# Performance work log

Hardware: AMD Instinct MI355X
Metric: run time of the kernel (lower is better)

Reference implementation:

```python
import jax, jax.numpy as jnp
import numpy as np

EPS = 1e-5

def _ln(x, g, b):
    mu = jnp.mean(x, axis=-1, keepdims=True)
    var = jnp.var(x, axis=-1, keepdims=True)
    return (x - mu) * jax.lax.rsqrt(var + EPS) * g + b

def setup_inputs() -> dict:
    B, N, D, H = 8, 1024, 1024, 16
    hid = 4 * D
    key = jax.random.key(0)
    ks = jax.random.split(key, 16)
    s = lambda fan_in: 1.0 / np.sqrt(fan_in)
    return {
        "x": jax.random.normal(ks[0], (B, N, D), jnp.float32),
        "ln1_g": jnp.ones((D,), jnp.float32),
        "ln1_b": jnp.zeros((D,), jnp.float32),
        "qkv_w": jax.random.normal(ks[1], (D, 3 * D), jnp.float32) * s(D),
        "qkv_b": jnp.zeros((3 * D,), jnp.float32),
        "proj_w": jax.random.normal(ks[2], (D, D), jnp.float32) * s(D),
        "proj_b": jnp.zeros((D,), jnp.float32),
        "ls1_g": jnp.full((D,), 1e-5, jnp.float32),
        "ln2_g": jnp.ones((D,), jnp.float32),
        "ln2_b": jnp.zeros((D,), jnp.float32),
        "fc1_w": jax.random.normal(ks[3], (D, hid), jnp.float32) * s(D),
        "fc1_b": jnp.zeros((hid,), jnp.float32),
        "fc2_w": jax.random.normal(ks[4], (hid, D), jnp.float32) * s(hid),
        "fc2_b": jnp.zeros((D,), jnp.float32),
        "ls2_g": jnp.full((D,), 1e-5, jnp.float32),
    }

def reference(x, ln1_g, ln1_b, qkv_w, qkv_b, proj_w, proj_b, ls1_g,
              ln2_g, ln2_b, fc1_w, fc1_b, fc2_w, fc2_b, ls2_g):
    B, N, D = x.shape
    H = 16
    hd = D // H
    scale = hd ** -0.5
    # --- attention branch (pre-norm) ---
    h = _ln(x, ln1_g, ln1_b)
    qkv = h @ qkv_w + qkv_b                      # [B,N,3D]
    q, k, v = jnp.split(qkv, 3, axis=-1)
    reshape = lambda t: t.reshape(B, N, H, hd).transpose(0, 2, 1, 3)  # [B,H,N,hd]
    q, k, v = reshape(q), reshape(k), reshape(v)
    attn = jax.nn.softmax(jnp.einsum('bhnd,bhmd->bhnm', q, k) * scale, axis=-1)
    o = jnp.einsum('bhnm,bhmd->bhnd', attn, v)
    o = o.transpose(0, 2, 1, 3).reshape(B, N, D)
    o = o @ proj_w + proj_b
    x = x + ls1_g * o
    # --- MLP branch (pre-norm) ---
    h = _ln(x, ln2_g, ln2_b)
    h = jax.nn.gelu(h @ fc1_w + fc1_b, approximate=False)
    h = h @ fc2_w + fc2_b
    x = x + ls2_g * h
    return x
```

## Files before the change

### kernel.cpp

```cpp
#include <hip/hip_runtime.h>
#include <hip/hip_bf16.h>
#include <cstdint>

using u16 = unsigned short;
using u8 = unsigned char;
typedef __attribute__((ext_vector_type(8))) short bf16x8;
typedef __attribute__((ext_vector_type(4))) float f32x4;
typedef __attribute__((ext_vector_type(16))) float f32x16;
typedef __attribute__((ext_vector_type(8))) int i32x8;
typedef __attribute__((ext_vector_type(4))) u16 u16x4;

#define MFMA_BF16(a, b, c) __builtin_amdgcn_mfma_f32_16x16x32_bf16((a), (b), (c), 0, 0, 0)
#define MFMA_FP8(a, b, c) \
  __builtin_amdgcn_mfma_scale_f32_32x32x64_f8f6f4((a), (b), (c), 0, 0, 0, 0x7f7f7f7f, 0, 0x7f7f7f7f)

__device__ __forceinline__ u16 f2bf(float f) {
  __hip_bfloat16 h = __float2bfloat16(f);
  return __builtin_bit_cast(u16, h);
}

__device__ __forceinline__ u8 f2fp8(float a) {
  int r = __builtin_amdgcn_cvt_pk_fp8_f32(a, a, 0, false);
  return (u8)(r & 0xff);
}

__device__ __forceinline__ uint32_t f2fp8x4(float a, float b, float c, float d) {
  int r = __builtin_amdgcn_cvt_pk_fp8_f32(a, b, 0, false);
  r = __builtin_amdgcn_cvt_pk_fp8_f32(c, d, r, true);
  return (uint32_t)r;
}

__device__ __forceinline__ void gl_lds16(const void* gsrc, void* ldst) {
  __builtin_amdgcn_global_load_lds(
      (__attribute__((address_space(1))) void*)const_cast<void*>(gsrc),
      (__attribute__((address_space(3))) void*)ldst, 16, 0, 0);
}

__global__ __launch_bounds__(256) void transpose_conv8(const float* __restrict__ src,
                                                       u8* __restrict__ dst, int K, int N) {
  __shared__ float t[32][33];
  const int bx = blockIdx.x, by = blockIdx.y;
  const int tid = threadIdx.x;
  const int r = tid >> 3, c = (tid & 7) * 4;
  const float4 v = *(const float4*)&src[(size_t)(by * 32 + r) * N + bx * 32 + c];
  t[r][c] = v.x; t[r][c + 1] = v.y; t[r][c + 2] = v.z; t[r][c + 3] = v.w;
  __syncthreads();
  uint32_t o = f2fp8x4(t[c][r], t[c + 1][r], t[c + 2][r], t[c + 3][r]);
  *(uint32_t*)&dst[(size_t)(bx * 32 + r) * K + by * 32 + c] = o;
}

__global__ __launch_bounds__(256) void ln_kernel(const float* __restrict__ x, const float* __restrict__ g,
                                                 const float* __restrict__ b, u8* __restrict__ out) {
  const int row = blockIdx.x, tid = threadIdx.x;
  const float* xr = x + (size_t)row * 1024;
  float4 v = *(const float4*)&xr[tid * 4];
  float s = v.x + v.y + v.z + v.w;
  float s2 = v.x * v.x + v.y * v.y + v.z * v.z + v.w * v.w;
#pragma unroll
  for (int off = 32; off; off >>= 1) { s += __shfl_xor(s, off); s2 += __shfl_xor(s2, off); }
  __shared__ float ps[4], ps2[4];
  const int wave = tid >> 6;
  if ((tid & 63) == 0) { ps[wave] = s; ps2[wave] = s2; }
  __syncthreads();
  s = ps[0] + ps[1] + ps[2] + ps[3];
  s2 = ps2[0] + ps2[1] + ps2[2] + ps2[3];
  const float mu = s * (1.0f / 1024.0f);
  const float var = s2 * (1.0f / 1024.0f) - mu * mu;
  const float rs = rsqrtf(var + 1e-5f);
  float4 gv = *(const float4*)&g[tid * 4];
  float4 bv = *(const float4*)&b[tid * 4];
  uint32_t o = f2fp8x4((v.x - mu) * rs * gv.x + bv.x, (v.y - mu) * rs * gv.y + bv.y,
                       (v.z - mu) * rs * gv.z + bv.z, (v.w - mu) * rs * gv.w + bv.w);
  *(uint32_t*)&out[(size_t)row * 1024 + tid * 4] = o;
}

__device__ __forceinline__ i32x8 ld_frag8(const u8* S, int row, int kk, int lk, int sw) {
  const int c0 = kk * 4 + lk * 2;
  const u8* rp = S + row * 128;
  int4 lo = *(const int4*)(rp + ((c0 ^ sw) * 16));
  int4 hi = *(const int4*)(rp + (((c0 + 1) ^ sw) * 16));
  i32x8 r = {lo.x, lo.y, lo.z, lo.w, hi.x, hi.y, hi.z, hi.w};
  return r;
}

template <int EPI>
__global__ __launch_bounds__(256, 3) void gemm_f8(const u8* __restrict__ A, const u8* __restrict__ Bt,
                                                  const float* __restrict__ bias, const float* __restrict__ xres,
                                                  const float* __restrict__ ls, float* __restrict__ outf,
                                                  u16* __restrict__ outh, u8* __restrict__ out8,
                                                  u16* __restrict__ vt_out, int M, int N, int K) {
  __shared__ __attribute__((aligned(16))) u8 As[128 * 128];
  __shared__ __attribute__((aligned(16))) u8 Bs[128 * 128];
  const int tid = threadIdx.x;
  const int w = tid >> 6, l = tid & 63;
  const int wr = w >> 1, wc = w & 1;
  const int l31 = l & 31, lk = l >> 5, sw = l & 7;
  const int bm = blockIdx.x, bn = blockIdx.y;

  f32x16 acc[2][2];
#pragma unroll
  for (int mi = 0; mi < 2; mi++)
#pragma unroll
    for (int ni = 0; ni < 2; ni++)
#pragma unroll
      for (int r = 0; r < 16; r++) acc[mi][ni][r] = 0.f;

  const int srow = w * 8 + (l >> 3);
  const int schunk = ((l & 7) ^ (l >> 3)) * 16;
  const u8* Ag = A + (size_t)(bm * 128 + srow) * K + schunk;
  const u8* Bg = Bt + (size_t)(bn * 128 + srow) * K + schunk;
  u8* Asw = &As[w * 1024];
  u8* Bsw = &Bs[w * 1024];
  const size_t row32K = (size_t)32 * K;

  for (int kt = 0; kt < K; kt += 128) {
    __syncthreads();
#pragma unroll
    for (int i = 0; i < 4; i++) gl_lds16(Ag + i * row32K + kt, Asw + i * 4096);
#pragma unroll
    for (int i = 0; i < 4; i++) gl_lds16(Bg + i * row32K + kt, Bsw + i * 4096);
    __syncthreads();
#pragma unroll
    for (int kk = 0; kk < 2; kk++) {
      i32x8 af[2], bf[2];
#pragma unroll
      for (int mi = 0; mi < 2; mi++) af[mi] = ld_frag8(As, wr * 64 + mi * 32 + l31, kk, lk, sw);
#pragma unroll
      for (int ni = 0; ni < 2; ni++) bf[ni] = ld_frag8(Bs, wc * 64 + ni * 32 + l31, kk, lk, sw);
#pragma unroll
      for (int mi = 0; mi < 2; mi++)
#pragma unroll
        for (int ni = 0; ni < 2; ni++) acc[mi][ni] = MFMA_FP8(af[mi], bf[ni], acc[mi][ni]);
    }
  }

  const int row0 = bm * 128 + wr * 64 + lk * 4;
  const int col0 = bn * 128 + wc * 64 + l31;
  if constexpr (EPI == 0) {
#pragma unroll
    for (int mi = 0; mi < 2; mi++)
#pragma unroll
      for (int ni = 0; ni < 2; ni++) {
        const int c = col0 + ni * 32;
        const float bs = bias[c];
        if (c < 2048) {
          const float scl = (c < 1024) ? 0.18033688011f : 1.0f;
#pragma unroll
          for (int reg = 0; reg < 16; reg++) {
            const int r = row0 + mi * 32 + (reg & 3) + 8 * (reg >> 2);
            outh[(size_t)r * N + c] = f2bf((acc[mi][ni][reg] + bs) * scl);
          }
        } else {
          const int cc = c - 2048;
          const int rb = row0 + mi * 32;
          u16* dst = vt_out + (size_t)((rb >> 10) * 16 + (cc >> 6)) * 65536 + (size_t)(cc & 63) * 1024;
          const int tok0 = rb & 1023;
#pragma unroll
          for (int rq = 0; rq < 4; rq++) {
            u16x4 pk;
#pragma unroll
            for (int j = 0; j < 4; j++) pk[j] = f2bf(acc[mi][ni][rq * 4 + j] + bs);
            *(u16x4*)&dst[tok0 + 8 * rq] = pk;
          }
        }
      }
  } else {
#pragma unroll
    for (int mi = 0; mi < 2; mi++)
#pragma unroll
      for (int ni = 0; ni < 2; ni++)
#pragma unroll
        for (int reg = 0; reg < 16; reg++) {
          const int r = row0 + mi * 32 + (reg & 3) + 8 * (reg >> 2);
          const int c = col0 + ni * 32;
          float v = acc[mi][ni][reg];
          if constexpr (EPI == 1) {
            const size_t idx = (size_t)r * N + c;
            outf[idx] = xres[idx] + ls[c] * (v + bias[c]);
          } else if constexpr (EPI == 2) {
            v += bias[c];
            const float x2 = v * v;
            const float u = v * (2.3022147f + 0.10295364f * x2);
            const float pe = exp2f(-u);
            out8[(size_t)r * N + c] = f2fp8(v * __builtin_amdgcn_rcpf(1.0f + pe));
          } else {
            const size_t idx = (size_t)r * N + c;
            outf[idx] += ls[c] * (v + bias[c]);
          }
        }
  }
}

__global__ __launch_bounds__(512, 4) void attn_kernel(const u16* __restrict__ qkv, const u16* __restrict__ vt,
                                                      u8* __restrict__ o) {
  __shared__ __attribute__((aligned(16))) u16 S[24576];
  u16* Ks = S;
  u16* Vs = S + 8192;
  u16* PQ = S + 16384;
  const int tid = threadIdx.x;
  const int wave = tid >> 6, lane = tid & 63;
  const int lrow = lane & 15, lhi = lane >> 4;
  const int bh = blockIdx.x;
  const int qt = blockIdx.y;
  const int b = bh >> 4, h = bh & 15;
  const int swz8 = (lane & 7) ^ (lane >> 3);
  const int swz16 = (lane & 15) ^ ((wave * 4 + (lane >> 4)) & 15);

  {
    const u16* gq = qkv + (size_t)(b * 1024 + qt * 256 + wave * 32 + (lane >> 3)) * 3072 + h * 64 + swz8 * 8;
#pragma unroll
    for (int i = 0; i < 4; i++) gl_lds16(gq + (size_t)(i * 8) * 3072, &S[wave * 2048 + i * 512]);
  }
  __syncthreads();
  const int pq0 = (lhi ^ (lrow & 7)) * 8;
  bf16x8 qf[2][2];
#pragma unroll
  for (int qg = 0; qg < 2; qg++) {
    qf[qg][0] = *(const bf16x8*)&S[wave * 2048 + (qg * 16 + lrow) * 64 + pq0];
    qf[qg][1] = *(const bf16x8*)&S[wave * 2048 + (qg * 16 + lrow) * 64 + (pq0 ^ 32)];
  }
  asm volatile("s_waitcnt lgkmcnt(0)" ::: "memory");
  __builtin_amdgcn_sched_barrier(0);

  bf16x8 onesf;
#pragma unroll
  for (int j = 0; j < 8; j++) onesf[j] = (short)0x3F80;

  f32x4 oa[2][4];
  f32x4 lb[2];
  f32x4 zero = {0.f, 0.f, 0.f, 0.f};
#pragma unroll
  for (int qg = 0; qg < 2; qg++) {
    lb[qg] = zero;
#pragma unroll
    for (int i = 0; i < 4; i++) oa[qg][i] = zero;
  }

  const u16* kg = qkv + (size_t)(b * 1024 + wave * 16 + (lane >> 3)) * 3072 + 1024 + h * 64 + swz8 * 8;
  const u16* vg = vt + (size_t)bh * 65536 + (size_t)(wave * 4 + (lane >> 4)) * 1024 + swz16 * 8;

  for (int kt = 0; kt < 1024; kt += 128) {
    __syncthreads();
    gl_lds16(kg + (size_t)kt * 3072, &Ks[(wave * 16) * 64]);
    gl_lds16(kg + (size_t)(kt + 8) * 3072, &Ks[(wave * 16 + 8) * 64]);
    gl_lds16(vg + kt, &Vs[(wave * 4) * 128]);
    gl_lds16(vg + (size_t)32 * 1024 + kt, &Vs[(32 + wave * 4) * 128]);
    __syncthreads();

#pragma unroll
    for (int half = 0; half < 2; half++) {
#pragma unroll
      for (int qg = 0; qg < 2; qg++) {
        f32x4 sf[4];
#pragma unroll
        for (int n = 0; n < 4; n++) sf[n] = zero;
#pragma unroll
        for (int n = 0; n < 4; n++) {
          bf16x8 kf0 = *(const bf16x8*)&Ks[(half * 64 + n * 16 + lrow) * 64 + pq0];
          bf16x8 kf1 = *(const bf16x8*)&Ks[(half * 64 + n * 16 + lrow) * 64 + (pq0 ^ 32)];
          sf[n] = MFMA_BF16(kf0, qf[qg][0], sf[n]);
          sf[n] = MFMA_BF16(kf1, qf[qg][1], sf[n]);
        }

#pragma unroll
        for (int n = 0; n < 4; n++) {
          u16x4 pk;
#pragma unroll
          for (int i = 0; i < 4; i++) pk[i] = f2bf(exp2f(sf[n][i]));
          const int c = 2 * n + (lhi >> 1);
          *(u16x4*)&PQ[wave * 1024 + lrow * 64 + ((c ^ (lrow & 7)) * 8) + (lhi & 1) * 4] = pk;
        }

        __builtin_amdgcn_s_setprio(1);
#pragma unroll
        for (int ks = 0; ks < 2; ks++) {
          bf16x8 pf = *(const bf16x8*)&PQ[wave * 1024 + lrow * 64 + (((ks * 4 + lhi) ^ (lrow & 7)) * 8)];
          lb[qg] = MFMA_BF16(pf, onesf, lb[qg]);
#pragma unroll
          for (int n2 = 0; n2 < 4; n2++) {
            bf16x8 vf =
                *(const bf16x8*)&Vs[(n2 * 16 + lrow) * 128 + (((half * 8 + ks * 4 + lhi) ^ lrow) * 8)];
            oa[qg][n2] = MFMA_BF16(pf, vf, oa[qg][n2]);
          }
        }
        __builtin_amdgcn_s_setprio(0);
      }
    }
  }

#pragma unroll
  for (int qg = 0; qg < 2; qg++) {
    float lq[4];
#pragma unroll
    for (int i = 0; i < 4; i++) lq[i] = 1.0f / lb[qg][i];
#pragma unroll
    for (int n2 = 0; n2 < 4; n2++)
#pragma unroll
      for (int i = 0; i < 4; i++) {
        const int tok = qt * 256 + wave * 32 + qg * 16 + lhi * 4 + i;
        o[(size_t)(b * 1024 + tok) * 1024 + h * 64 + n2 * 16 + lrow] = f2fp8(oa[qg][n2][i] * lq[i]);
      }
  }
}

extern "C" void kernel_launch(void* const* d_in, const int* in_sizes, int n_in, void* d_out, int out_size,
                              void* d_ws, size_t ws_size, hipStream_t stream) {
  const float* x = (const float*)d_in[0];
  const float* ln1_g = (const float*)d_in[1];
  const float* ln1_b = (const float*)d_in[2];
  const float* qkv_w = (const float*)d_in[3];
  const float* qkv_b = (const float*)d_in[4];
  const float* proj_w = (const float*)d_in[5];
  const float* proj_b = (const float*)d_in[6];
  const float* ls1_g = (const float*)d_in[7];
  const float* ln2_g = (const float*)d_in[8];
  const float* ln2_b = (const float*)d_in[9];
  const float* fc1_w = (const float*)d_in[10];
  const float* fc1_b = (const float*)d_in[11];
  const float* fc2_w = (const float*)d_in[12];
  const float* fc2_b = (const float*)d_in[13];
  const float* ls2_g = (const float*)d_in[14];
  float* out = (float*)d_out;

  u8* p = (u8*)d_ws;
  u8* wq8 = p;  p += (size_t)3072 * 1024;
  u8* wp8 = p;  p += (size_t)1024 * 1024;
  u8* wf18 = p; p += (size_t)4096 * 1024;
  u8* wf28 = p; p += (size_t)1024 * 4096;
  u8* hbuf8 = p; p += (size_t)8192 * 1024;
  u16* qkvb = (u16*)p; p += (size_t)8192 * 3072 * 2;
  u16* vtb = (u16*)p;  p += (size_t)128 * 64 * 1024 * 2;
  u8* ob8 = p;  p += (size_t)8192 * 1024;
  u8* hid8 = (u8*)qkvb;

  transpose_conv8<<<dim3(96, 32), 256, 0, stream>>>(qkv_w, wq8, 1024, 3072);
  transpose_conv8<<<dim3(32, 32), 256, 0, stream>>>(proj_w, wp8, 1024, 1024);
  transpose_conv8<<<dim3(128, 32), 256, 0, stream>>>(fc1_w, wf18, 1024, 4096);
  transpose_conv8<<<dim3(32, 128), 256, 0, stream>>>(fc2_w, wf28, 4096, 1024);

  ln_kernel<<<8192, 256, 0, stream>>>(x, ln1_g, ln1_b, hbuf8);
  gemm_f8<0><<<dim3(64, 24), 256, 0, stream>>>(hbuf8, wq8, qkv_b, nullptr, nullptr, nullptr, qkvb, nullptr,
                                               vtb, 8192, 3072, 1024);
  attn_kernel<<<dim3(128, 4), 512, 0, stream>>>(qkvb, vtb, ob8);
  gemm_f8<1><<<dim3(64, 8), 256, 0, stream>>>(ob8, wp8, proj_b, x, ls1_g, out, nullptr, nullptr, nullptr,
                                              8192, 1024, 1024);
  ln_kernel<<<8192, 256, 0, stream>>>(out, ln2_g, ln2_b, hbuf8);
  gemm_f8<2><<<dim3(64, 32), 256, 0, stream>>>(hbuf8, wf18, fc1_b, nullptr, nullptr, nullptr, nullptr, hid8,
                                               nullptr, 8192, 4096, 1024);
  gemm_f8<3><<<dim3(64, 8), 256, 0, stream>>>(hid8, wf28, fc2_b, nullptr, ls2_g, out, nullptr, nullptr,
                                              nullptr, 8192, 1024, 4096);
}
```

Before: 249.8 us.

## Double-buffer K/V tiles in LDS to overlap loads with attention compute

The attention kernel now keeps two K/V LDS buffers and prefetches the next 128-key tile while computing on the current one, using explicit vmcnt waits and barriers in place of the two full __syncthreads per iteration. Q staging moves to a separate LDS region that the second K/V buffer later reuses. The goal is to hide global-load latency behind MFMA work. In exchange, LDS use rises from 48KB to 80KB per block, which may lower occupancy below the declared 4 blocks per CU.

Result: no change. 253.3 us (+1.4%).

```diff
diff --git a/kernel.cpp b/kernel.cpp
--- a/kernel.cpp
+++ b/kernel.cpp
@@ -193,10 +193,7 @@
 
 __global__ __launch_bounds__(512, 4) void attn_kernel(const u16* __restrict__ qkv, const u16* __restrict__ vt,
                                                       u8* __restrict__ o) {
-  __shared__ __attribute__((aligned(16))) u16 S[24576];
-  u16* Ks = S;
-  u16* Vs = S + 8192;
-  u16* PQ = S + 16384;
+  __shared__ __attribute__((aligned(16))) u16 S[40960];
   const int tid = threadIdx.x;
   const int wave = tid >> 6, lane = tid & 63;
   const int lrow = lane & 15, lhi = lane >> 4;
@@ -205,19 +202,32 @@
   const int b = bh >> 4, h = bh & 15;
   const int swz8 = (lane & 7) ^ (lane >> 3);
   const int swz16 = (lane & 15) ^ ((wave * 4 + (lane >> 4)) & 15);
+  const int pqb = 32768 + wave * 1024;
+
+  const u16* kg = qkv + (size_t)(b * 1024 + wave * 16 + (lane >> 3)) * 3072 + 1024 + h * 64 + swz8 * 8;
+  const u16* vg = vt + (size_t)bh * 65536 + (size_t)(wave * 4 + (lane >> 4)) * 1024 + swz16 * 8;
+
+  auto stageKV = [&](int tk, int bb) {
+    gl_lds16(kg + (size_t)(tk * 128) * 3072, &S[bb * 16384 + (wave * 16) * 64]);
+    gl_lds16(kg + (size_t)(tk * 128 + 8) * 3072, &S[bb * 16384 + (wave * 16 + 8) * 64]);
+    gl_lds16(vg + tk * 128, &S[bb * 16384 + 8192 + (wave * 4) * 128]);
+    gl_lds16(vg + (size_t)32 * 1024 + tk * 128, &S[bb * 16384 + 8192 + (32 + wave * 4) * 128]);
+  };
 
   {
     const u16* gq = qkv + (size_t)(b * 1024 + qt * 256 + wave * 32 + (lane >> 3)) * 3072 + h * 64 + swz8 * 8;
 #pragma unroll
-    for (int i = 0; i < 4; i++) gl_lds16(gq + (size_t)(i * 8) * 3072, &S[wave * 2048 + i * 512]);
-  }
-  __syncthreads();
+    for (int i = 0; i < 4; i++) gl_lds16(gq + (size_t)(i * 8) * 3072, &S[16384 + wave * 2048 + i * 512]);
+  }
+  stageKV(0, 0);
+  asm volatile("s_waitcnt vmcnt(4)" ::: "memory");
+  __builtin_amdgcn_s_barrier();
   const int pq0 = (lhi ^ (lrow & 7)) * 8;
   bf16x8 qf[2][2];
 #pragma unroll
   for (int qg = 0; qg < 2; qg++) {
-    qf[qg][0] = *(const bf16x8*)&S[wave * 2048 + (qg * 16 + lrow) * 64 + pq0];
-    qf[qg][1] = *(const bf16x8*)&S[wave * 2048 + (qg * 16 + lrow) * 64 + (pq0 ^ 32)];
+    qf[qg][0] = *(const bf16x8*)&S[16384 + wave * 2048 + (qg * 16 + lrow) * 64 + pq0];
+    qf[qg][1] = *(const bf16x8*)&S[16384 + wave * 2048 + (qg * 16 + lrow) * 64 + (pq0 ^ 32)];
   }
   asm volatile("s_waitcnt lgkmcnt(0)" ::: "memory");
   __builtin_amdgcn_sched_barrier(0);
@@ -236,16 +246,18 @@
     for (int i = 0; i < 4; i++) oa[qg][i] = zero;
   }
 
-  const u16* kg = qkv + (size_t)(b * 1024 + wave * 16 + (lane >> 3)) * 3072 + 1024 + h * 64 + swz8 * 8;
-  const u16* vg = vt + (size_t)bh * 65536 + (size_t)(wave * 4 + (lane >> 4)) * 1024 + swz16 * 8;
-
-  for (int kt = 0; kt < 1024; kt += 128) {
-    __syncthreads();
-    gl_lds16(kg + (size_t)kt * 3072, &Ks[(wave * 16) * 64]);
-    gl_lds16(kg + (size_t)(kt + 8) * 3072, &Ks[(wave * 16 + 8) * 64]);
-    gl_lds16(vg + kt, &Vs[(wave * 4) * 128]);
-    gl_lds16(vg + (size_t)32 * 1024 + kt, &Vs[(32 + wave * 4) * 128]);
-    __syncthreads();
+  for (int t = 0; t < 8; ++t) {
+    const int cur = t & 1;
+    const int kvb = cur * 16384;
+    asm volatile("s_waitcnt lgkmcnt(0)" ::: "memory");
+    __builtin_amdgcn_s_barrier();
+    if (t < 7) {
+      stageKV(t + 1, cur ^ 1);
+      asm volatile("s_waitcnt vmcnt(4)" ::: "memory");
+    } else {
+      asm volatile("s_waitcnt vmcnt(0)" ::: "memory");
+    }
+    __builtin_amdgcn_s_barrier();
 
 #pragma unroll
     for (int half = 0; half < 2; half++) {
@@ -256,8 +268,8 @@
         for (int n = 0; n < 4; n++) sf[n] = zero;
 #pragma unroll
         for (int n = 0; n < 4; n++) {
-          bf16x8 kf0 = *(const bf16x8*)&Ks[(half * 64 + n * 16 + lrow) * 64 + pq0];
-          bf16x8 kf1 = *(const bf16x8*)&Ks[(half * 64 + n * 16 + lrow) * 64 + (pq0 ^ 32)];
+          bf16x8 kf0 = *(const bf16x8*)&S[kvb + (half * 64 + n * 16 + lrow) * 64 + pq0];
+          bf16x8 kf1 = *(const bf16x8*)&S[kvb + (half * 64 + n * 16 + lrow) * 64 + (pq0 ^ 32)];
           sf[n] = MFMA_BF16(kf0, qf[qg][0], sf[n]);
           sf[n] = MFMA_BF16(kf1, qf[qg][1], sf[n]);
         }
@@ -268,18 +280,18 @@
 #pragma unroll
           for (int i = 0; i < 4; i++) pk[i] = f2bf(exp2f(sf[n][i]));
           const int c = 2 * n + (lhi >> 1);
-          *(u16x4*)&PQ[wave * 1024 + lrow * 64 + ((c ^ (lrow & 7)) * 8) + (lhi & 1) * 4] = pk;
+          *(u16x4*)&S[pqb + lrow * 64 + ((c ^ (lrow & 7)) * 8) + (lhi & 1) * 4] = pk;
         }
 
         __builtin_amdgcn_s_setprio(1);
 #pragma unroll
         for (int ks = 0; ks < 2; ks++) {
-          bf16x8 pf = *(const bf16x8*)&PQ[wave * 1024 + lrow * 64 + (((ks * 4 + lhi) ^ (lrow & 7)) * 8)];
+          bf16x8 pf = *(const bf16x8*)&S[pqb + lrow * 64 + (((ks * 4 + lhi) ^ (lrow & 7)) * 8)];
           lb[qg] = MFMA_BF16(pf, onesf, lb[qg]);
 #pragma unroll
           for (int n2 = 0; n2 < 4; n2++) {
-            bf16x8 vf =
-                *(const bf16x8*)&Vs[(n2 * 16 + lrow) * 128 + (((half * 8 + ks * 4 + lhi) ^ lrow) * 8)];
+            bf16x8 vf = *(const bf16x8*)&S[kvb + 8192 + (n2 * 16 + lrow) * 128 +
+                                           (((half * 8 + ks * 4 + lhi) ^ lrow) * 8)];
             oa[qg][n2] = MFMA_BF16(pf, vf, oa[qg][n2]);
           }
         }
```
